# Kernel optimization log

Measured on AMD Instinct MI355X. Metric: run time of the kernel, lower is better.

The kernel has to match this reference:

```python
import jax, jax.numpy as jnp
import numpy as np

SPATIAL_SHAPES = [(128, 128), (64, 64), (32, 32), (16, 16)]
D_MODEL = 256
N_HEADS = 8
N_LEVELS = 4
N_POINTS = 4
HEAD_DIM = D_MODEL // N_HEADS
B = 2
LEN_Q = sum(h * w for h, w in SPATIAL_SHAPES)  # 21760
LEN_IN = LEN_Q


def setup_inputs() -> dict:
    key = jax.random.key(0)
    ks = jax.random.split(key, 11)
    s = 1.0 / np.sqrt(D_MODEL).astype(np.float32)
    query = jax.random.normal(ks[0], (B, LEN_Q, D_MODEL), jnp.float32)
    reference_points = jax.random.uniform(ks[1], (B, LEN_Q, N_LEVELS, 2), jnp.float32)
    input_flatten = jax.random.normal(ks[2], (B, LEN_IN, D_MODEL), jnp.float32)
    W_off = jax.random.normal(ks[3], (D_MODEL, N_HEADS * N_LEVELS * N_POINTS * 2), jnp.float32) * s
    b_off = jnp.zeros((N_HEADS * N_LEVELS * N_POINTS * 2,), jnp.float32)
    W_attn = jax.random.normal(ks[4], (D_MODEL, N_HEADS * N_LEVELS * N_POINTS), jnp.float32) * s
    b_attn = jnp.zeros((N_HEADS * N_LEVELS * N_POINTS,), jnp.float32)
    W_val = jax.random.normal(ks[5], (D_MODEL, D_MODEL), jnp.float32) * s
    b_val = jnp.zeros((D_MODEL,), jnp.float32)
    W_out = jax.random.normal(ks[6], (D_MODEL, D_MODEL), jnp.float32) * s
    b_out = jnp.zeros((D_MODEL,), jnp.float32)
    return {"query": query, "reference_points": reference_points, "input_flatten": input_flatten,
            "W_off": W_off, "b_off": b_off, "W_attn": W_attn, "b_attn": b_attn,
            "W_val": W_val, "b_val": b_val, "W_out": W_out, "b_out": b_out}


def _ms_deform_core(value, sampling_locations, attention_weights):
    # value: (B, H, Dh, N_total); sampling_locations: (B, Lq, H, L, P, 2) in [0,1]
    # attention_weights: (B, Lq, H, L*P)
    Bv, Hn, Dh, _ = value.shape
    Lq = sampling_locations.shape[1]
    P = sampling_locations.shape[4]
    BN = Bv * Hn
    grids = 2.0 * sampling_locations - 1.0
    splits = np.cumsum([h * w for h, w in SPATIAL_SHAPES])[:-1].tolist()
    value_list = jnp.split(value, splits, axis=3)
    sampled_levels = []
    for lid, (Hh, Ww) in enumerate(SPATIAL_SHAPES):
        # (BN, H*W, Dh)
        val_flat = jnp.transpose(value_list[lid].reshape(BN, Dh, Hh * Ww), (0, 2, 1))
        # (BN, Lq, P, 2)
        g = jnp.transpose(grids[:, :, :, lid, :, :], (0, 2, 1, 3, 4)).reshape(BN, Lq, P, 2)
        ix = ((g[..., 0] + 1.0) * Ww - 1.0) / 2.0
        iy = ((g[..., 1] + 1.0) * Hh - 1.0) / 2.0
        ix0 = jnp.floor(ix).astype(jnp.int32)
        iy0 = jnp.floor(iy).astype(jnp.int32)
        ix1 = ix0 + 1
        iy1 = iy0 + 1
        fx = (ix - ix0.astype(ix.dtype))[..., None]
        fy = (iy - iy0.astype(iy.dtype))[..., None]

        def valid(yy, xx):
            return ((xx >= 0) & (xx < Ww) & (yy >= 0) & (yy < Hh)).astype(val_flat.dtype)[..., None]

        def gather(yy, xx):
            idx = (jnp.clip(yy, 0, Hh - 1) * Ww + jnp.clip(xx, 0, Ww - 1)).reshape(BN, Lq * P)
            out = jnp.take_along_axis(val_flat, idx[:, :, None], axis=1)
            return out.reshape(BN, Lq, P, Dh)

        v00 = gather(iy0, ix0) * valid(iy0, ix0)
        v01 = gather(iy0, ix1) * valid(iy0, ix1)
        v10 = gather(iy1, ix0) * valid(iy1, ix0)
        v11 = gather(iy1, ix1) * valid(iy1, ix1)
        sampled = ((1 - fx) * (1 - fy) * v00 + fx * (1 - fy) * v01
                   + (1 - fx) * fy * v10 + fx * fy * v11)  # (BN, Lq, P, Dh)
        sampled_levels.append(jnp.transpose(sampled, (0, 3, 1, 2)))  # (BN, Dh, Lq, P)
    # (BN, Dh, Lq, L*P)
    sv = jnp.stack(sampled_levels, axis=-2).reshape(BN, Dh, Lq, N_LEVELS * P)
    attn = jnp.transpose(attention_weights, (0, 2, 1, 3)).reshape(BN, 1, Lq, N_LEVELS * P)
    out = jnp.sum(sv * attn, axis=-1)  # (BN, Dh, Lq)
    out = out.reshape(Bv, Hn * Dh, Lq)
    return jnp.transpose(out, (0, 2, 1))  # (B, Lq, d_model)


def reference(query, reference_points, input_flatten, W_off, b_off, W_attn, b_attn, W_val, b_val, W_out, b_out):
    Bq, Lq, _ = query.shape
    Len_in = input_flatten.shape[1]
    value = input_flatten @ W_val + b_val  # (B, Len_in, d_model)
    offsets = (query @ W_off + b_off).reshape(Bq, Lq, N_HEADS, N_LEVELS, N_POINTS, 2)
    attn = jax.nn.softmax((query @ W_attn + b_attn).reshape(Bq, Lq, N_HEADS, N_LEVELS * N_POINTS), axis=-1)
    # normalizer is (W, H) per level
    offset_normalizer = jnp.asarray([[w, h] for h, w in SPATIAL_SHAPES], dtype=query.dtype)
    sampling_locations = (reference_points[:, :, None, :, None, :]
                          + offsets / offset_normalizer[None, None, None, :, None, :])
    value = jnp.transpose(value, (0, 2, 1)).reshape(Bq, N_HEADS, HEAD_DIM, Len_in)
    out = _ms_deform_core(value, sampling_locations, attn)
    return out @ W_out + b_out
```

## Files before the change

kernel.cpp:

```cpp
#include <hip/hip_runtime.h>
#include <hip/hip_bf16.h>
#include <hip/hip_fp16.h>
#include <type_traits>

#define B_    2
#define LQ_   21760
#define LEN_  21760
#define DM    256
#define NH    8
#define NL    4
#define NP    4
#define HD    32

#define WS_VAL   0u
#define WS_SAMP  22282240u
#define WS_OA    44564480u
#define WS_WT    77987840u

typedef __attribute__((ext_vector_type(4))) float f32x4;
typedef __attribute__((ext_vector_type(8))) short bf16x8;
typedef __attribute__((ext_vector_type(4))) unsigned int u32x4;
typedef __attribute__((ext_vector_type(2))) unsigned int u32x2;

__device__ __forceinline__ unsigned short f2bf(float v) {
    __hip_bfloat16 h = __float2bfloat16(v);
    return *reinterpret_cast<unsigned short*>(&h);
}
__device__ __forceinline__ unsigned int pk2bf(float a, float b) {
    return (unsigned int)f2bf(a) | ((unsigned int)f2bf(b) << 16);
}
__device__ __forceinline__ unsigned int pk2h(float a, float b) {
    __half2 h = __floats2half2_rn(a, b);
    union { __half2 h; unsigned int u; } c; c.h = h; return c.u;
}
__device__ __forceinline__ __half2 u2h2(unsigned int u) {
    union { unsigned int u; __half2 h; } c; c.u = u; return c.h;
}

__device__ __forceinline__ void gload16(u32x4& d, const char* p) {
    asm volatile("global_load_dwordx4 %0, %1, off" : "=v"(d) : "v"(p));
}

__global__ __launch_bounds__(256) void wt_cvt_all(const float* __restrict__ Wv,
                                                  const float* __restrict__ Wo,
                                                  const float* __restrict__ Wa,
                                                  const float* __restrict__ Wu,
                                                  unsigned short* __restrict__ wt) {
    const float* Ws[4] = {Wv, Wo, Wa, Wu};
    const int Ns[4] = {256, 256, 128, 256};
    const unsigned int dof[4] = {0u, 65536u, 131072u, 163840u};
    const int m = blockIdx.z;
    const int n0 = blockIdx.x * 16, k0 = blockIdx.y * 16;
    if (n0 >= Ns[m]) return;
    __shared__ float tile[16][17];
    const int tx = threadIdx.x & 15, ty = threadIdx.x >> 4;
    tile[ty][tx] = Ws[m][(size_t)(k0 + ty) * Ns[m] + n0 + tx];
    __syncthreads();
    wt[dof[m] + (size_t)(n0 + ty) * 256 + k0 + tx] = f2bf(tile[tx][ty]);
}

__global__ __launch_bounds__(256) void gemm_pre(const float* __restrict__ inpf,
                                                const float* __restrict__ query,
                                                const unsigned short* __restrict__ Wt_val,
                                                const unsigned short* __restrict__ Wt_oa,
                                                const float* __restrict__ b_val,
                                                const float* __restrict__ b_off,
                                                const float* __restrict__ b_attn,
                                                unsigned short* __restrict__ val_h,
                                                unsigned short* __restrict__ oa_h) {
    __shared__ unsigned short As[128 * 32];
    __shared__ unsigned short Bs[128 * 32];
    const int t = threadIdx.x;
    const int wv = t >> 6;
    const int ln = t & 63;
    const int job = (blockIdx.x >= 2);
    const int n0 = (job ? (blockIdx.x - 2) : blockIdx.x) * 128;
    const int m0 = blockIdx.y * 128;
    const float* A = job ? query : inpf;
    const unsigned short* Bt = job ? Wt_oa : Wt_val;
    const int K = 256;
    const int wm = (wv & 1) * 64;
    const int wn = (wv >> 1) * 64;
    const int lrow = ln & 15;
    const int kq = ln >> 4;

    f32x4 acc[4][4] = {};

    for (int k0 = 0; k0 < K; k0 += 32) {
#pragma unroll
        for (int c = 0; c < 4; ++c) {
            const int i = t + c * 256;
            const int row = i >> 3;
            const int kq4 = (i & 7) * 4;
            f32x4 v = *(const f32x4*)&A[(size_t)(m0 + row) * K + k0 + kq4];
            uint2 p = make_uint2(pk2bf(v.x, v.y), pk2bf(v.z, v.w));
            *(uint2*)((char*)As + row * 64 + kq4 * 2) = p;
        }
#pragma unroll
        for (int c = 0; c < 2; ++c) {
            const int o = c * 4096 + t * 16;
            const int row = o >> 6;
            const int ke = (o & 63) >> 1;
            const unsigned short* gb = Bt + (size_t)(n0 + row) * K + k0 + ke;
            __builtin_amdgcn_global_load_lds(
                (const __attribute__((address_space(1))) void*)gb,
                (__attribute__((address_space(3))) void*)((char*)Bs + o), 16, 0, 0);
        }
        __syncthreads();

        bf16x8 af[4], bfr[4];
#pragma unroll
        for (int i = 0; i < 4; ++i) {
            af[i]  = *(const bf16x8*)((char*)As + (wm + i * 16 + lrow) * 64 + kq * 16);
            bfr[i] = *(const bf16x8*)((char*)Bs + (wn + i * 16 + lrow) * 64 + kq * 16);
        }
#pragma unroll
        for (int i = 0; i < 4; ++i)
#pragma unroll
            for (int j = 0; j < 4; ++j)
                acc[i][j] = __builtin_amdgcn_mfma_f32_16x16x32_bf16(af[i], bfr[j], acc[i][j], 0, 0, 0);
        __syncthreads();
    }

    const int b = m0 / LQ_;
#pragma unroll
    for (int j = 0; j < 4; ++j) {
        const int n = n0 + wn + j * 16 + lrow;
        const float bb = job ? ((n < 256) ? b_off[n] : b_attn[n - 256]) : b_val[n];
#pragma unroll
        for (int i = 0; i < 4; ++i) {
            const int mrow = m0 + wm + i * 16 + kq * 4;
#pragma unroll
            for (int r = 0; r < 4; ++r) {
                const float v = acc[i][j][r] + bb;
                const unsigned short hv = (unsigned short)__half_as_ushort(__float2half(v));
                if (job) {
                    oa_h[(size_t)(mrow + r) * 384 + n] = hv;
                } else {
                    const int pix = (mrow + r) - b * LQ_;
                    const int h = n >> 5, c = n & 31;
                    val_h[((size_t)(b * NH + h) * LQ_ + pix) * HD + c] = hv;
                }
            }
        }
    }
}

__global__ __launch_bounds__(256) void gemm_out(const unsigned short* __restrict__ Ab,
                                                const unsigned short* __restrict__ Bt,
                                                const float* __restrict__ bias,
                                                float* __restrict__ C) {
    __shared__ unsigned short As[128 * 32];
    __shared__ unsigned short Bs[128 * 32];
    const int t = threadIdx.x;
    const int wv = t >> 6;
    const int ln = t & 63;
    const int n0 = blockIdx.x * 128;
    const int m0 = blockIdx.y * 128;
    const int N = 256, K = 256;
    const int wm = (wv & 1) * 64;
    const int wn = (wv >> 1) * 64;
    const int lrow = ln & 15;
    const int kq = ln >> 4;

    f32x4 acc[4][4] = {};

    for (int k0 = 0; k0 < K; k0 += 32) {
#pragma unroll
        for (int c = 0; c < 2; ++c) {
            const int o = c * 4096 + t * 16;
            const int row = o >> 6;
            const int ke = (o & 63) >> 1;
            const unsigned short* ga = Ab + (size_t)(m0 + row) * K + k0 + ke;
            const unsigned short* gb = Bt + (size_t)(n0 + row) * K + k0 + ke;
            __builtin_amdgcn_global_load_lds(
                (const __attribute__((address_space(1))) void*)ga,
                (__attribute__((address_space(3))) void*)((char*)As + o), 16, 0, 0);
            __builtin_amdgcn_global_load_lds(
                (const __attribute__((address_space(1))) void*)gb,
                (__attribute__((address_space(3))) void*)((char*)Bs + o), 16, 0, 0);
        }
        __syncthreads();

        bf16x8 af[4], bfr[4];
#pragma unroll
        for (int i = 0; i < 4; ++i) {
            af[i]  = *(const bf16x8*)((char*)As + (wm + i * 16 + lrow) * 64 + kq * 16);
            bfr[i] = *(const bf16x8*)((char*)Bs + (wn + i * 16 + lrow) * 64 + kq * 16);
        }
#pragma unroll
        for (int i = 0; i < 4; ++i)
#pragma unroll
            for (int j = 0; j < 4; ++j)
                acc[i][j] = __builtin_amdgcn_mfma_f32_16x16x32_bf16(af[i], bfr[j], acc[i][j], 0, 0, 0);
        __syncthreads();
    }

#pragma unroll
    for (int j = 0; j < 4; ++j) {
        const int n = n0 + wn + j * 16 + lrow;
        const float bb = bias[n];
#pragma unroll
        for (int i = 0; i < 4; ++i) {
            const int mrow = m0 + wm + i * 16 + kq * 4;
#pragma unroll
            for (int r = 0; r < 4; ++r)
                C[(size_t)(mrow + r) * N + n] = acc[i][j][r] + bb;
        }
    }
}

#define QB6 32

#define MSDA_VMWAIT(n) { asm volatile("s_waitcnt vmcnt(" #n ")" ::: "memory"); \
                         __builtin_amdgcn_sched_barrier(0); }

#define MSDA_ISSUE(i) u32x4 va_##i, vc_##i; { \
    const u32x2 xy = *(const u32x2*)&s_pkw[wb ^ ((i) << 2)]; \
    gload16(va_##i, vbase + (size_t)xy[0] * 64); \
    gload16(vc_##i, vbase + (size_t)xy[1] * 64); }

#define MSDA_CONSUME(i) { \
    const u32x2 zw = *(const u32x2*)&s_pkw[(wb ^ ((i) << 2)) + 2]; \
    const __half2 w0 = u2h2(__builtin_amdgcn_perm(zw[0], zw[0], wsel)); \
    const __half2 w1 = u2h2(__builtin_amdgcn_perm(zw[1], zw[1], wsel)); \
    ah0 = __hfma2(w0, u2h2(va_##i[0]), ah0); \
    ah1 = __hfma2(w0, u2h2(va_##i[1]), ah1); \
    ah2 = __hfma2(w0, u2h2(va_##i[2]), ah2); \
    ah3 = __hfma2(w0, u2h2(va_##i[3]), ah3); \
    ah0 = __hfma2(w1, u2h2(vc_##i[0]), ah0); \
    ah1 = __hfma2(w1, u2h2(vc_##i[1]), ah1); \
    ah2 = __hfma2(w1, u2h2(vc_##i[2]), ah2); \
    ah3 = __hfma2(w1, u2h2(vc_##i[3]), ah3); }

#define MSDA_FLUSH() { \
    float2 f0 = __half22float2(ah0); facc0 += f0.x; facc1 += f0.y; ah0 = u2h2(0u); \
    float2 f1 = __half22float2(ah1); facc2 += f1.x; facc3 += f1.y; ah1 = u2h2(0u); \
    float2 f2 = __half22float2(ah2); facc4 += f2.x; facc5 += f2.y; ah2 = u2h2(0u); \
    float2 f3 = __half22float2(ah3); facc6 += f3.x; facc7 += f3.y; ah3 = u2h2(0u); }

__global__ __launch_bounds__(256) void msda_sample8(const unsigned short* __restrict__ value,
                                                    const unsigned short* __restrict__ oa,
                                                    const float* __restrict__ refp,
                                                    unsigned short* __restrict__ samp) {
    __shared__ __align__(16) char smem[9216];
    unsigned int* s_pkw = (unsigned int*)smem;
    float* s_off   = (float*)smem;
    float* s_logit = (float*)(smem + 4096);
    float* s_aw    = (float*)(smem + 6144);
    float* s_ref   = (float*)(smem + 8192);

    const int t = threadIdx.x;
    const int j = blockIdx.x;
    const int h = j & 7;
    const int bqc = j >> 3;
    const int b = (bqc >= 680);
    const int q0 = (bqc - b * 680) * QB6;
    const int bq0 = b * LQ_ + q0;

    {
        const int q = t >> 3, c = t & 7;
        const unsigned short* oab = oa + (size_t)(bq0 + q) * 384;
        u32x2 r0 = __builtin_nontemporal_load((const u32x2*)(oab + h * 32) + c);
        float2 f0 = __half22float2(u2h2(r0.x));
        float2 f1 = __half22float2(u2h2(r0.y));
        f32x4 o0 = {f0.x, f0.y, f1.x, f1.y};
        ((f32x4*)s_off)[q * 8 + c] = o0;
        unsigned int r1 = __builtin_nontemporal_load((const unsigned int*)(oab + 256 + h * 16) + c);
        float2 g0 = __half22float2(u2h2(r1));
        ((float2*)s_logit)[q * 8 + c] = make_float2(g0.x, g0.y);
        s_ref[q * 8 + c] = __builtin_nontemporal_load(refp + (size_t)(bq0 + q) * 8 + c);
    }
    __syncthreads();

    if (t < 32) {
        const float* lg = s_logit + t * 16;
        float m = -1e30f;
#pragma unroll
        for (int i = 0; i < 16; ++i) m = fmaxf(m, lg[i]);
        float e[16], s = 0.f;
#pragma unroll
        for (int i = 0; i < 16; ++i) { e[i] = __expf(lg[i] - m); s += e[i]; }
        const float inv = 1.f / s;
#pragma unroll
        for (int i = 0; i < 16; ++i) s_aw[t * 16 + i] = e[i] * inv;
    }
    __syncthreads();

    uint4 ent[2];
    int wrd[2];
    {
        const int Wls[4] = {128, 64, 32, 16};
        const int Hls[4] = {128, 64, 32, 16};
        const int st_[4] = {0, 16384, 20480, 21504};
#pragma unroll
        for (int ii = 0; ii < 2; ++ii) {
            const int s = t * 2 + ii;
            const int q = s >> 4;
            const int lp = s & 15;
            const int l = lp >> 2;
            const int Wl = Wls[l], Hl = Hls[l], base = st_[l];
            const float ix = s_ref[q * 8 + l * 2]     * (float)Wl - 0.5f + s_off[q * 32 + lp * 2];
            const float iy = s_ref[q * 8 + l * 2 + 1] * (float)Hl - 0.5f + s_off[q * 32 + lp * 2 + 1];
            const float fix = floorf(ix), fiy = floorf(iy);
            const int x0 = (int)fix, y0 = (int)fiy;
            const float fx = ix - fix, fy = iy - fiy;
            int sx; float wl, wr;
            if (x0 < 0)            { sx = 0;      wl = (x0 == -1) ? fx : 0.f;        wr = 0.f; }
            else if (x0 >= Wl - 1) { sx = Wl - 2; wl = 0.f; wr = (x0 == Wl - 1) ? (1.f - fx) : 0.f; }
            else                   { sx = x0;     wl = 1.f - fx;                     wr = fx; }
            const float g0 = ((y0 >= 0) & (y0 < Hl)) ? (1.f - fy) : 0.f;
            const float g1 = ((y0 + 1 >= 0) & (y0 + 1 < Hl)) ? fy : 0.f;
            const int cy0 = min(max(y0, 0), Hl - 1);
            const int cy1 = min(max(y0 + 1, 0), Hl - 1);
            const float aw = s_aw[q * 16 + lp];
            ent[ii].x = (unsigned int)(base + cy0 * Wl + sx);
            ent[ii].y = (unsigned int)(base + cy1 * Wl + sx);
            ent[ii].z = pk2h(aw * wl * g0, aw * wr * g0);
            ent[ii].w = pk2h(aw * wl * g1, aw * wr * g1);
            wrd[ii] = q * 64 + ((lp ^ (q & 7)) << 2);
        }
    }
    __syncthreads();

#pragma unroll
    for (int ii = 0; ii < 2; ++ii)
        *(uint4*)&s_pkw[wrd[ii]] = ent[ii];
    __syncthreads();

    const int lane = t & 63;
    const int wv = t >> 6;
    const int ql = lane >> 3;
    const int q = wv * 8 + ql;
    const int dg = lane & 7;
    const char* vbase = (const char*)(value + ((size_t)(b * NH + h) * LQ_) * HD) + dg * 16;
    const unsigned int wsel = (dg < 4) ? 0x01000100u : 0x03020302u;
    const int wb = q * 64 + (ql << 2);

    float facc0 = 0.f, facc1 = 0.f, facc2 = 0.f, facc3 = 0.f;
    float facc4 = 0.f, facc5 = 0.f, facc6 = 0.f, facc7 = 0.f;
    __half2 ah0 = u2h2(0u), ah1 = u2h2(0u), ah2 = u2h2(0u), ah3 = u2h2(0u);

    MSDA_ISSUE(0)  MSDA_ISSUE(1)  MSDA_ISSUE(2)  MSDA_ISSUE(3)
    MSDA_ISSUE(4)  MSDA_ISSUE(5)  MSDA_ISSUE(6)  MSDA_ISSUE(7)
    MSDA_VMWAIT(8)
    MSDA_ISSUE(8)  MSDA_ISSUE(9)  MSDA_ISSUE(10) MSDA_ISSUE(11)
    MSDA_CONSUME(0) MSDA_CONSUME(1) MSDA_CONSUME(2) MSDA_CONSUME(3)
    MSDA_FLUSH()
    MSDA_VMWAIT(8)
    MSDA_ISSUE(12) MSDA_ISSUE(13) MSDA_ISSUE(14) MSDA_ISSUE(15)
    MSDA_CONSUME(4) MSDA_CONSUME(5) MSDA_CONSUME(6) MSDA_CONSUME(7)
    MSDA_FLUSH()
    MSDA_VMWAIT(8)
    MSDA_CONSUME(8) MSDA_CONSUME(9) MSDA_CONSUME(10) MSDA_CONSUME(11)
    MSDA_FLUSH()
    MSDA_VMWAIT(0)
    MSDA_CONSUME(12) MSDA_CONSUME(13) MSDA_CONSUME(14) MSDA_CONSUME(15)
    MSDA_FLUSH()

    facc0 += __shfl_xor(facc0, 4);
    facc1 += __shfl_xor(facc1, 4);
    facc2 += __shfl_xor(facc2, 4);
    facc3 += __shfl_xor(facc3, 4);
    facc4 += __shfl_xor(facc4, 4);
    facc5 += __shfl_xor(facc5, 4);
    facc6 += __shfl_xor(facc6, 4);
    facc7 += __shfl_xor(facc7, 4);

    if (dg < 4) {
        u32x4 o;
        o.x = pk2bf(facc0, facc1);
        o.y = pk2bf(facc2, facc3);
        o.z = pk2bf(facc4, facc5);
        o.w = pk2bf(facc6, facc7);
        __builtin_nontemporal_store(o, (u32x4*)(samp + (size_t)(bq0 + q) * 256 + h * HD + dg * 8));
    }
}

extern "C" void kernel_launch(void* const* d_in, const int* in_sizes, int n_in,
                              void* d_out, int out_size, void* d_ws, size_t ws_size,
                              hipStream_t stream) {
    const float* query  = (const float*)d_in[0];
    const float* refp   = (const float*)d_in[1];
    const float* inpf   = (const float*)d_in[2];
    const float* W_off  = (const float*)d_in[3];
    const float* b_off  = (const float*)d_in[4];
    const float* W_attn = (const float*)d_in[5];
    const float* b_attn = (const float*)d_in[6];
    const float* W_val  = (const float*)d_in[7];
    const float* b_val  = (const float*)d_in[8];
    const float* W_out  = (const float*)d_in[9];
    const float* b_out  = (const float*)d_in[10];
    float* out = (float*)d_out;

    char* ws = (char*)d_ws;
    unsigned short* val_h   = (unsigned short*)(ws + WS_VAL);
    unsigned short* samp_bf = (unsigned short*)(ws + WS_SAMP);
    unsigned short* oa_h    = (unsigned short*)(ws + WS_OA);
    unsigned short* wt      = (unsigned short*)(ws + WS_WT);
    unsigned short* Wt_val  = wt;
    unsigned short* Wt_oa   = wt + 65536;
    unsigned short* Wt_out  = wt + 163840;

    const int M = B_ * LQ_;

    wt_cvt_all<<<dim3(16, 16, 4), 256, 0, stream>>>(W_val, W_off, W_attn, W_out, wt);

    gemm_pre<<<dim3(5, M / 128), 256, 0, stream>>>(
        inpf, query, Wt_val, Wt_oa, b_val, b_off, b_attn, val_h, oa_h);

    msda_sample8<<<dim3(B_ * NH * (LQ_ / QB6)), 256, 0, stream>>>(val_h, oa_h, refp, samp_bf);

    gemm_out<<<dim3(2, M / 128), 256, 0, stream>>>(samp_bf, Wt_out, b_out, out);
}
```

Measured before the change: 279.6 us.

## Fuse offset and attention-logit projection into the sampling kernel

New measurement: 350.9 us. +25.5%, slower.

```diff
diff --git a/kernel.cpp b/kernel.cpp
--- a/kernel.cpp
+++ b/kernel.cpp
@@ -14,8 +14,7 @@
 
 #define WS_VAL   0u
 #define WS_SAMP  22282240u
-#define WS_OA    44564480u
-#define WS_WT    77987840u
+#define WS_WT    44564480u
 
 typedef __attribute__((ext_vector_type(4))) float f32x4;
 typedef __attribute__((ext_vector_type(8))) short bf16x8;
@@ -59,25 +58,17 @@
     wt[dof[m] + (size_t)(n0 + ty) * 256 + k0 + tx] = f2bf(tile[tx][ty]);
 }
 
-__global__ __launch_bounds__(256) void gemm_pre(const float* __restrict__ inpf,
-                                                const float* __restrict__ query,
+__global__ __launch_bounds__(256) void gemm_val(const float* __restrict__ inpf,
                                                 const unsigned short* __restrict__ Wt_val,
-                                                const unsigned short* __restrict__ Wt_oa,
                                                 const float* __restrict__ b_val,
-                                                const float* __restrict__ b_off,
-                                                const float* __restrict__ b_attn,
-                                                unsigned short* __restrict__ val_h,
-                                                unsigned short* __restrict__ oa_h) {
+                                                unsigned short* __restrict__ val_h) {
     __shared__ unsigned short As[128 * 32];
     __shared__ unsigned short Bs[128 * 32];
     const int t = threadIdx.x;
     const int wv = t >> 6;
     const int ln = t & 63;
-    const int job = (blockIdx.x >= 2);
-    const int n0 = (job ? (blockIdx.x - 2) : blockIdx.x) * 128;
+    const int n0 = blockIdx.x * 128;
     const int m0 = blockIdx.y * 128;
-    const float* A = job ? query : inpf;
-    const unsigned short* Bt = job ? Wt_oa : Wt_val;
     const int K = 256;
     const int wm = (wv & 1) * 64;
     const int wn = (wv >> 1) * 64;
@@ -92,7 +83,7 @@
             const int i = t + c * 256;
             const int row = i >> 3;
             const int kq4 = (i & 7) * 4;
-            f32x4 v = *(const f32x4*)&A[(size_t)(m0 + row) * K + k0 + kq4];
+            f32x4 v = *(const f32x4*)&inpf[(size_t)(m0 + row) * K + k0 + kq4];
             uint2 p = make_uint2(pk2bf(v.x, v.y), pk2bf(v.z, v.w));
             *(uint2*)((char*)As + row * 64 + kq4 * 2) = p;
         }
@@ -101,7 +92,7 @@
             const int o = c * 4096 + t * 16;
             const int row = o >> 6;
             const int ke = (o & 63) >> 1;
-            const unsigned short* gb = Bt + (size_t)(n0 + row) * K + k0 + ke;
+            const unsigned short* gb = Wt_val + (size_t)(n0 + row) * K + k0 + ke;
             __builtin_amdgcn_global_load_lds(
                 (const __attribute__((address_space(1))) void*)gb,
                 (__attribute__((address_space(3))) void*)((char*)Bs + o), 16, 0, 0);
@@ -126,7 +117,7 @@
 #pragma unroll
     for (int j = 0; j < 4; ++j) {
         const int n = n0 + wn + j * 16 + lrow;
-        const float bb = job ? ((n < 256) ? b_off[n] : b_attn[n - 256]) : b_val[n];
+        const float bb = b_val[n];
 #pragma unroll
         for (int i = 0; i < 4; ++i) {
             const int mrow = m0 + wm + i * 16 + kq * 4;
@@ -134,13 +125,9 @@
             for (int r = 0; r < 4; ++r) {
                 const float v = acc[i][j][r] + bb;
                 const unsigned short hv = (unsigned short)__half_as_ushort(__float2half(v));
-                if (job) {
-                    oa_h[(size_t)(mrow + r) * 384 + n] = hv;
-                } else {
-                    const int pix = (mrow + r) - b * LQ_;
-                    const int h = n >> 5, c = n & 31;
-                    val_h[((size_t)(b * NH + h) * LQ_ + pix) * HD + c] = hv;
-                }
+                const int pix = (mrow + r) - b * LQ_;
+                const int hh = n >> 5, c = n & 31;
+                val_h[((size_t)(b * NH + hh) * LQ_ + pix) * HD + c] = hv;
             }
         }
     }
@@ -239,16 +226,21 @@
     float2 f2 = __half22float2(ah2); facc4 += f2.x; facc5 += f2.y; ah2 = u2h2(0u); \
     float2 f3 = __half22float2(ah3); facc6 += f3.x; facc7 += f3.y; ah3 = u2h2(0u); }
 
-__global__ __launch_bounds__(256) void msda_sample8(const unsigned short* __restrict__ value,
-                                                    const unsigned short* __restrict__ oa,
+__global__ __launch_bounds__(256) void msda_sample9(const unsigned short* __restrict__ value,
+                                                    const unsigned short* __restrict__ wt_oa,
+                                                    const float* __restrict__ b_off,
+                                                    const float* __restrict__ b_attn,
+                                                    const float* __restrict__ query,
                                                     const float* __restrict__ refp,
                                                     unsigned short* __restrict__ samp) {
-    __shared__ __align__(16) char smem[9216];
-    unsigned int* s_pkw = (unsigned int*)smem;
-    float* s_off   = (float*)smem;
-    float* s_logit = (float*)(smem + 4096);
-    float* s_aw    = (float*)(smem + 6144);
-    float* s_ref   = (float*)(smem + 8192);
+    __shared__ __align__(16) char smem[25600];
+    unsigned short* s_qt = (unsigned short*)smem;
+    float* s_part = (float*)smem;
+    float* s_off   = (float*)(smem + 16384);
+    float* s_logit = (float*)(smem + 20480);
+    float* s_aw    = (float*)(smem + 22528);
+    unsigned int* s_pkw = (unsigned int*)(smem + 16384);
+    float* s_ref   = (float*)(smem + 24576);
 
     const int t = threadIdx.x;
     const int j = blockIdx.x;
@@ -257,19 +249,70 @@
     const int b = (bqc >= 680);
     const int q0 = (bqc - b * 680) * QB6;
     const int bq0 = b * LQ_ + q0;
+    const int lane = t & 63;
+    const int wv = t >> 6;
 
     {
         const int q = t >> 3, c = t & 7;
-        const unsigned short* oab = oa + (size_t)(bq0 + q) * 384;
-        u32x2 r0 = __builtin_nontemporal_load((const u32x2*)(oab + h * 32) + c);
-        float2 f0 = __half22float2(u2h2(r0.x));
-        float2 f1 = __half22float2(u2h2(r0.y));
-        f32x4 o0 = {f0.x, f0.y, f1.x, f1.y};
-        ((f32x4*)s_off)[q * 8 + c] = o0;
-        unsigned int r1 = __builtin_nontemporal_load((const unsigned int*)(oab + 256 + h * 16) + c);
-        float2 g0 = __half22float2(u2h2(r1));
-        ((float2*)s_logit)[q * 8 + c] = make_float2(g0.x, g0.y);
+        const float* qrow = query + (size_t)(bq0 + q) * 256 + c * 32;
+        const int rb = q * 512;
+        const int sw = (q & 7) << 4;
+#pragma unroll
+        for (int v = 0; v < 4; ++v) {
+            f32x4 x0 = *(const f32x4*)(qrow + v * 8);
+            f32x4 x1 = *(const f32x4*)(qrow + v * 8 + 4);
+            u32x4 p;
+            p.x = pk2bf(x0.x, x0.y); p.y = pk2bf(x0.z, x0.w);
+            p.z = pk2bf(x1.x, x1.y); p.w = pk2bf(x1.z, x1.w);
+            *(u32x4*)((char*)s_qt + rb + ((c * 64 + v * 16) ^ sw)) = p;
+        }
         s_ref[q * 8 + c] = __builtin_nontemporal_load(refp + (size_t)(bq0 + q) * 8 + c);
+    }
+    __syncthreads();
+
+    {
+        const int mt = wv & 1;
+        const int kh = wv >> 1;
+        const int lr = lane & 15, kq = lane >> 4;
+        const int arow = mt * 16 + lr;
+        const int abase = arow * 512;
+        const int asw = (arow & 7) << 4;
+        const unsigned short* bt0 = wt_oa + ((size_t)(h * 32) + lr) * 256;
+        const unsigned short* bt1 = wt_oa + ((size_t)(h * 32 + 16) + lr) * 256;
+        const unsigned short* bt2 = wt_oa + ((size_t)(256 + h * 16) + lr) * 256;
+        f32x4 acc0 = {0.f, 0.f, 0.f, 0.f}, acc1 = acc0, acc2 = acc0;
+#pragma unroll
+        for (int s = 0; s < 4; ++s) {
+            const int k = kh * 128 + s * 32 + kq * 8;
+            bf16x8 af  = *(const bf16x8*)((char*)s_qt + abase + ((k * 2) ^ asw));
+            bf16x8 bf0 = *(const bf16x8*)(bt0 + k);
+            bf16x8 bf1 = *(const bf16x8*)(bt1 + k);
+            bf16x8 bf2 = *(const bf16x8*)(bt2 + k);
+            acc0 = __builtin_amdgcn_mfma_f32_16x16x32_bf16(af, bf0, acc0, 0, 0, 0);
+            acc1 = __builtin_amdgcn_mfma_f32_16x16x32_bf16(af, bf1, acc1, 0, 0, 0);
+            acc2 = __builtin_amdgcn_mfma_f32_16x16x32_bf16(af, bf2, acc2, 0, 0, 0);
+        }
+        __syncthreads();
+        float* pb = s_part + kh * 1536;
+#pragma unroll
+        for (int r = 0; r < 4; ++r) {
+            const int q = mt * 16 + kq * 4 + r;
+            pb[q * 48 + lr]      = acc0[r];
+            pb[q * 48 + 16 + lr] = acc1[r];
+            pb[q * 48 + 32 + lr] = acc2[r];
+        }
+    }
+    __syncthreads();
+
+#pragma unroll
+    for (int e = 0; e < 6; ++e) {
+        const int idx = t + e * 256;
+        const int q = (idx * 1366) >> 16;
+        const int n = idx - q * 48;
+        const float v = s_part[q * 48 + n] + s_part[1536 + q * 48 + n]
+                      + ((n < 32) ? b_off[h * 32 + n] : b_attn[h * 16 + n - 32]);
+        if (n < 32) s_off[q * 32 + n] = v;
+        else        s_logit[q * 16 + n - 32] = v;
     }
     __syncthreads();
 
@@ -328,8 +371,6 @@
         *(uint4*)&s_pkw[wrd[ii]] = ent[ii];
     __syncthreads();
 
-    const int lane = t & 63;
-    const int wv = t >> 6;
     const int ql = lane >> 3;
     const int q = wv * 8 + ql;
     const int dg = lane & 7;
@@ -396,7 +437,6 @@
     char* ws = (char*)d_ws;
     unsigned short* val_h   = (unsigned short*)(ws + WS_VAL);
     unsigned short* samp_bf = (unsigned short*)(ws + WS_SAMP);
-    unsigned short* oa_h    = (unsigned short*)(ws + WS_OA);
     unsigned short* wt      = (unsigned short*)(ws + WS_WT);
     unsigned short* Wt_val  = wt;
     unsigned short* Wt_oa   = wt + 65536;
@@ -406,10 +446,10 @@
 
     wt_cvt_all<<<dim3(16, 16, 4), 256, 0, stream>>>(W_val, W_off, W_attn, W_out, wt);
 
-    gemm_pre<<<dim3(5, M / 128), 256, 0, stream>>>(
-        inpf, query, Wt_val, Wt_oa, b_val, b_off, b_attn, val_h, oa_h);
-
-    msda_sample8<<<dim3(B_ * NH * (LQ_ / QB6)), 256, 0, stream>>>(val_h, oa_h, refp, samp_bf);
+    gemm_val<<<dim3(2, M / 128), 256, 0, stream>>>(inpf, Wt_val, b_val, val_h);
+
+    msda_sample9<<<dim3(B_ * NH * (LQ_ / QB6)), 256, 0, stream>>>(
+        val_h, Wt_oa, b_off, b_attn, query, refp, samp_bf);
 
     gemm_out<<<dim3(2, M / 128), 256, 0, stream>>>(samp_bf, Wt_out, b_out, out);
 }
```
